# Kernel optimization log

Hardware: AMD Instinct MI355X
Metric: run time of the kernel (lower is better)

The kernel has to match this reference:

```python
import jax, jax.numpy as jnp
import numpy as np

CHEB_K = 3  # from init_kwargs


def setup_inputs() -> dict:
    key = jax.random.key(0)
    k1, k2, k3, k4 = jax.random.split(key, 4)
    B, N, C_IN, C_OUT, D = 32, 4096, 32, 64, 16
    x = jax.random.normal(k1, (B, N, C_IN), dtype=jnp.float32)
    node_embeddings = jax.random.normal(k2, (N, D), dtype=jnp.float32)
    laplacian_mx = jnp.zeros((N, N), dtype=jnp.float32)  # unused by forward
    weights_pool = jax.random.normal(k3, (D, CHEB_K, C_IN, C_OUT), dtype=jnp.float32) * 0.1
    bias_pool = jax.random.normal(k4, (D, C_OUT), dtype=jnp.float32) * 0.1
    return {
        'x': x,
        'node_embeddings': node_embeddings,
        'laplacian_mx': laplacian_mx,
        'weights_pool': weights_pool,
        'bias_pool': bias_pool,
    }


def reference(x, node_embeddings, laplacian_mx, weights_pool, bias_pool):
    N = node_embeddings.shape[0]
    # adaptive adjacency: softmax(relu(E E^T)) over rows
    supports = jax.nn.softmax(jax.nn.relu(node_embeddings @ node_embeddings.T), axis=1)
    # Chebyshev recursion T_0=I, T_1=A, T_k = 2A T_{k-1} - T_{k-2}
    support_set = [jnp.eye(N, dtype=x.dtype), supports]
    for _ in range(2, CHEB_K):
        support_set.append(2.0 * supports @ support_set[-1] - support_set[-2])
    supports_k = jnp.stack(support_set, axis=0)  # [K, N, N]
    # per-node generated weights/bias
    weights = jnp.einsum('nd,dkio->nkio', node_embeddings, weights_pool)  # [N,K,I,O]
    bias = node_embeddings @ bias_pool  # [N, O]
    # graph propagation: [K,N,N] x [B,N,I] -> [B,K,N,I] -> [B,N,K,I]
    x_g = jnp.einsum('knm,bmc->bknc', supports_k, x).transpose(0, 2, 1, 3)
    # per-node grouped GEMM
    out = jnp.einsum('bnki,nkio->bno', x_g, weights) + bias
    return out
```

## Files before the change

kernel.cpp:

```cpp
#include <hip/hip_runtime.h>
#include <hip/hip_bf16.h>

#define N_NODES 4096
#define BATCH   32
#define CIN     32
#define COUT    64
#define DEMB    16
#define NCOL    (BATCH * CIN)
#define KIO     (3 * CIN * COUT)
#define SPLITK  4

typedef __bf16 bf16x8 __attribute__((ext_vector_type(8)));
typedef float  floatx4 __attribute__((ext_vector_type(4)));

__device__ inline void load_lds16(const void* g, void* l) {
    __builtin_amdgcn_global_load_lds(
        (const __attribute__((address_space(1))) void*)g,
        (__attribute__((address_space(3))) void*)l, 16, 0, 0);
}

__global__ __launch_bounds__(256) void compute_U_kernel(
        const float* __restrict__ E, __hip_bfloat16* __restrict__ U,
        float* __restrict__ invRow) {
    const int n0   = blockIdx.x * 8;
    const int t    = threadIdx.x;
    const int lane = t & 63, wave = t >> 6;
    __shared__ float red[4][8];

    float en[8][DEMB];
#pragma unroll
    for (int r = 0; r < 8; ++r) {
        const float4* er = (const float4*)&E[(size_t)(n0 + r) * DEMB];
        const float4 a0 = er[0], a1 = er[1], a2 = er[2], a3 = er[3];
        en[r][ 0]=a0.x; en[r][ 1]=a0.y; en[r][ 2]=a0.z; en[r][ 3]=a0.w;
        en[r][ 4]=a1.x; en[r][ 5]=a1.y; en[r][ 6]=a1.z; en[r][ 7]=a1.w;
        en[r][ 8]=a2.x; en[r][ 9]=a2.y; en[r][10]=a2.z; en[r][11]=a2.w;
        en[r][12]=a3.x; en[r][13]=a3.y; en[r][14]=a3.z; en[r][15]=a3.w;
    }

    float sum[8] = {0.f, 0.f, 0.f, 0.f, 0.f, 0.f, 0.f, 0.f};

    for (int tile = 0; tile < 16; ++tile) {
        const int c = tile * 256 + t;
        const float4* em4 = (const float4*)&E[(size_t)c * DEMB];
        const float4 b0 = em4[0], b1 = em4[1], b2 = em4[2], b3 = em4[3];
        float em[DEMB];
        em[ 0]=b0.x; em[ 1]=b0.y; em[ 2]=b0.z; em[ 3]=b0.w;
        em[ 4]=b1.x; em[ 5]=b1.y; em[ 6]=b1.z; em[ 7]=b1.w;
        em[ 8]=b2.x; em[ 9]=b2.y; em[10]=b2.z; em[11]=b2.w;
        em[12]=b3.x; em[13]=b3.y; em[14]=b3.z; em[15]=b3.w;
#pragma unroll
        for (int r = 0; r < 8; ++r) {
            float dt = 0.f;
#pragma unroll
            for (int d = 0; d < DEMB; ++d) dt += en[r][d] * em[d];
            const float ev = __expf(fmaxf(dt, 0.f));
            sum[r] += ev;
            U[(size_t)(n0 + r) * N_NODES + c] = __float2bfloat16(ev);
        }
    }
#pragma unroll
    for (int r = 0; r < 8; ++r)
#pragma unroll
        for (int off = 32; off > 0; off >>= 1) sum[r] += __shfl_xor(sum[r], off);
    if (lane == 0)
#pragma unroll
        for (int r = 0; r < 8; ++r) red[wave][r] = sum[r];
    __syncthreads();
    if (t < 8)
        invRow[n0 + t] = 1.0f / (red[0][t] + red[1][t] + red[2][t] + red[3][t]);
}

__global__ __launch_bounds__(256) void transpose_kernel(
        const float* __restrict__ x,
        __hip_bfloat16* __restrict__ Xt, __hip_bfloat16* __restrict__ Bt) {
    const int m0 = blockIdx.x * 64;
    const int b  = blockIdx.y;
    const int t  = threadIdx.x;
    __shared__ float tile[64][33];
    {
        const int ml = t >> 2, cg = (t & 3) * 8;
        const float* src = &x[((size_t)b * N_NODES + (m0 + ml)) * CIN + cg];
        const float4 r0 = *(const float4*)src;
        const float4 r1 = *(const float4*)(src + 4);
        tile[ml][cg+0] = r0.x; tile[ml][cg+1] = r0.y; tile[ml][cg+2] = r0.z; tile[ml][cg+3] = r0.w;
        tile[ml][cg+4] = r1.x; tile[ml][cg+5] = r1.y; tile[ml][cg+6] = r1.z; tile[ml][cg+7] = r1.w;
    }
    __syncthreads();
    {
        const int ml = t >> 2, cg = (t & 3) * 8;
        __hip_bfloat16* dst = &Xt[(size_t)(m0 + ml) * NCOL + b * CIN + cg];
#pragma unroll
        for (int j = 0; j < 8; ++j) dst[j] = __float2bfloat16(tile[ml][cg + j]);
    }
    {
        const int c = t >> 3, mg = (t & 7) * 8;
        __hip_bfloat16* dst = &Bt[(size_t)(b * CIN + c) * N_NODES + m0 + mg];
#pragma unroll
        for (int j = 0; j < 8; ++j) dst[j] = __float2bfloat16(tile[mg + j][c]);
    }
}

__global__ __launch_bounds__(256) void gen_w_kernel(
        const float* __restrict__ E, const float* __restrict__ Wp,
        __hip_bfloat16* __restrict__ Wn) {
    const int c   = blockIdx.x >> 3;
    const int oo0 = (blockIdx.x & 7) * 8;
    const int nc  = blockIdx.y * 64;
    const int t   = threadIdx.x;
    const int kk  = t & 31;
    const int oo  = oo0 + (t >> 5);

    __shared__ float et[64][DEMB];
    ((float4*)et)[t] = ((const float4*)&E[(size_t)nc * DEMB])[t];
    __syncthreads();

    const int srccol = (c * 32 + kk) * 64 + oo;
    float w[DEMB];
#pragma unroll
    for (int d = 0; d < DEMB; ++d) w[d] = Wp[(size_t)d * KIO + srccol];

    const int dstoff = c * 2048 + (oo >> 4) * 512 + (oo & 15) * 32 + kk;
    for (int nl = 0; nl < 64; ++nl) {
        float acc = 0.0f;
#pragma unroll
        for (int d = 0; d < DEMB; ++d) acc += et[nl][d] * w[d];
        Wn[(size_t)(nc + nl) * KIO + dstoff] = __float2bfloat16(acc);
    }
}

#define GBM 256
#define GBN 256
#define GBK 64

__global__ __launch_bounds__(512, 2) void gemm_splitk_kernel(
        const __hip_bfloat16* __restrict__ A,
        const __hip_bfloat16* __restrict__ Bt,
        __hip_bfloat16* __restrict__ P,
        int M, int NC, int K) {
    const int t    = threadIdx.x;
    const int row0 = blockIdx.x * GBM;
    const int col0 = blockIdx.y * GBN;
    const int z    = blockIdx.z;
    const int NT   = (K >> 6) / SPLITK;
    const int kb0  = z * NT * GBK;

    __shared__ alignas(16) __hip_bfloat16 As[2][16384];
    __shared__ alignas(16) __hip_bfloat16 Bs[2][16384];

    const int lane = t & 63, wave = t >> 6;
    const int l16 = lane & 15, quad = lane >> 4;
    const int wr = wave >> 2, wc = wave & 3;

    const int R0 = wr * 128 + l16;
    const int C0 = wc * 64 + l16;
    const int u_par = (l16 & 1) * 4 + quad;
    const int Aoff = (R0 >> 1) * 64 + ((u_par ^ ((R0 >> 1) & 7)) * 8);
    const int Boff = (C0 >> 1) * 64 + ((u_par ^ ((C0 >> 1) & 7)) * 8);

    auto stageA = [&](int buf, int kb, int kh, int s) {
        const int L = s * 512 + t;
        const int p = L >> 3, j = L & 7;
        const int u = j ^ (p & 7);
        const int rr = p * 2 + (u >> 2);
        const int qq = u & 3;
        load_lds16(&A[(size_t)(row0 + rr) * K + kb + kh * 32 + qq * 8],
                   &As[buf][(size_t)(kh * 1024 + L) * 8]);
    };
    auto stageB = [&](int buf, int kb, int kh, int s) {
        const int L = s * 512 + t;
        const int p = L >> 3, j = L & 7;
        const int u = j ^ (p & 7);
        const int rr = p * 2 + (u >> 2);
        const int qq = u & 3;
        load_lds16(&Bt[(size_t)(col0 + rr) * K + kb + kh * 32 + qq * 8],
                   &Bs[buf][(size_t)(kh * 1024 + L) * 8]);
    };

    floatx4 acc[8][4] = {};

#pragma unroll
    for (int s = 0; s < 2; ++s) stageA(0, kb0, 0, s);
#pragma unroll
    for (int s = 0; s < 2; ++s) stageB(0, kb0, 0, s);
#pragma unroll
    for (int s = 0; s < 2; ++s) stageA(0, kb0, 1, s);
#pragma unroll
    for (int s = 0; s < 2; ++s) stageB(0, kb0, 1, s);
#pragma unroll
    for (int s = 0; s < 2; ++s) stageA(1, kb0 + GBK, 0, s);
#pragma unroll
    for (int s = 0; s < 2; ++s) stageB(1, kb0 + GBK, 0, s);
    asm volatile("s_waitcnt vmcnt(4)" ::: "memory");
    __builtin_amdgcn_s_barrier();
    __builtin_amdgcn_sched_barrier(0);

    for (int tt = 0; tt < NT; ++tt) {
        const int buf = tt & 1;
        const int nb1 = (tt + 1) & 1;
        const int nb2 = buf;
        const int kb1 = kb0 + (tt + 1) * GBK;
        const int kb2 = kb0 + (tt + 2) * GBK;
        const bool g1 = (tt + 1 < NT), g2 = (tt + 2 < NT);

        bf16x8 bfrag[4], afrag[4];

#pragma unroll
        for (int n = 0; n < 4; ++n)
            bfrag[n] = *(const bf16x8*)&Bs[buf][n * 512 + Boff];
#pragma unroll
        for (int m = 0; m < 4; ++m)
            afrag[m] = *(const bf16x8*)&As[buf][m * 512 + Aoff];
        if (g1) { stageA(nb1, kb1, 1, 0); stageA(nb1, kb1, 1, 1); }
        __builtin_amdgcn_s_barrier();
        asm volatile("s_waitcnt lgkmcnt(0)" ::: "memory");
        __builtin_amdgcn_sched_barrier(0);
        __builtin_amdgcn_s_setprio(1);
#pragma unroll
        for (int m = 0; m < 4; ++m)
#pragma unroll
            for (int n = 0; n < 4; ++n)
                acc[m][n] = __builtin_amdgcn_mfma_f32_16x16x32_bf16(
                                afrag[m], bfrag[n], acc[m][n], 0, 0, 0);
        __builtin_amdgcn_s_setprio(0);
        __builtin_amdgcn_s_barrier();

#pragma unroll
        for (int m = 0; m < 4; ++m)
            afrag[m] = *(const bf16x8*)&As[buf][2048 + m * 512 + Aoff];
        if (g1) { stageB(nb1, kb1, 1, 0); stageB(nb1, kb1, 1, 1); }
        __builtin_amdgcn_s_barrier();
        asm volatile("s_waitcnt lgkmcnt(0)" ::: "memory");
        __builtin_amdgcn_sched_barrier(0);
        __builtin_amdgcn_s_setprio(1);
#pragma unroll
        for (int m = 0; m < 4; ++m)
#pragma unroll
            for (int n = 0; n < 4; ++n)
                acc[4 + m][n] = __builtin_amdgcn_mfma_f32_16x16x32_bf16(
                                    afrag[m], bfrag[n], acc[4 + m][n], 0, 0, 0);
        __builtin_amdgcn_s_setprio(0);
        __builtin_amdgcn_s_barrier();

#pragma unroll
        for (int n = 0; n < 4; ++n)
            bfrag[n] = *(const bf16x8*)&Bs[buf][8192 + n * 512 + Boff];
#pragma unroll
        for (int m = 0; m < 4; ++m)
            afrag[m] = *(const bf16x8*)&As[buf][8192 + m * 512 + Aoff];
        if (g2) { stageA(nb2, kb2, 0, 0); stageA(nb2, kb2, 0, 1); }
        __builtin_amdgcn_s_barrier();
        asm volatile("s_waitcnt lgkmcnt(0)" ::: "memory");
        __builtin_amdgcn_sched_barrier(0);
        __builtin_amdgcn_s_setprio(1);
#pragma unroll
        for (int m = 0; m < 4; ++m)
#pragma unroll
            for (int n = 0; n < 4; ++n)
                acc[m][n] = __builtin_amdgcn_mfma_f32_16x16x32_bf16(
                                afrag[m], bfrag[n], acc[m][n], 0, 0, 0);
        __builtin_amdgcn_s_setprio(0);
        __builtin_amdgcn_s_barrier();

#pragma unroll
        for (int m = 0; m < 4; ++m)
            afrag[m] = *(const bf16x8*)&As[buf][8192 + 2048 + m * 512 + Aoff];
        if (g2) { stageB(nb2, kb2, 0, 0); stageB(nb2, kb2, 0, 1); }
        __builtin_amdgcn_s_barrier();
        asm volatile("s_waitcnt lgkmcnt(0)" ::: "memory");
        __builtin_amdgcn_sched_barrier(0);
        __builtin_amdgcn_s_setprio(1);
#pragma unroll
        for (int m = 0; m < 4; ++m)
#pragma unroll
            for (int n = 0; n < 4; ++n)
                acc[4 + m][n] = __builtin_amdgcn_mfma_f32_16x16x32_bf16(
                                    afrag[m], bfrag[n], acc[4 + m][n], 0, 0, 0);
        __builtin_amdgcn_s_setprio(0);
        if (tt < NT - 2) asm volatile("s_waitcnt vmcnt(4)" ::: "memory");
        else             asm volatile("s_waitcnt vmcnt(0)" ::: "memory");
        __builtin_amdgcn_s_barrier();
        __builtin_amdgcn_sched_barrier(0);
    }

    __hip_bfloat16* Pz = P + (size_t)z * M * NC;
#pragma unroll
    for (int mq = 0; mq < 2; ++mq)
#pragma unroll
        for (int m = 0; m < 4; ++m)
#pragma unroll
            for (int n = 0; n < 4; ++n)
#pragma unroll
                for (int r = 0; r < 4; ++r) {
                    const int rg = row0 + wr * 128 + mq * 64 + m * 16 + quad * 4 + r;
                    const int cg = col0 + wc * 64 + n * 16 + l16;
                    Pz[(size_t)rg * NC + cg] = __float2bfloat16(acc[mq * 4 + m][n][r]);
                }
}

__global__ __launch_bounds__(256) void combine1_kernel(
        const __hip_bfloat16* __restrict__ P, const float* __restrict__ invRow,
        __hip_bfloat16* __restrict__ Y, __hip_bfloat16* __restrict__ Yt,
        int M, int NC) {
    const int c0 = blockIdx.x * 64, m0 = blockIdx.y * 64;
    const int t = threadIdx.x;
    __shared__ float tile[64][65];
    const size_t stride = (size_t)M * NC;
#pragma unroll
    for (int j = 0; j < 16; ++j) {
        const int lin = t + j * 256;
        const int r = lin >> 6, c = lin & 63;
        const size_t idx = (size_t)(m0 + r) * NC + c0 + c;
        float s = 0.f;
#pragma unroll
        for (int z = 0; z < SPLITK; ++z) s += __bfloat162float(P[idx + z * stride]);
        s *= invRow[m0 + r];
        tile[r][c] = s;
        Y[idx] = __float2bfloat16(s);
    }
    __syncthreads();
#pragma unroll
    for (int j = 0; j < 16; ++j) {
        const int lin = t + j * 256;
        const int c = lin >> 6, r = lin & 63;
        Yt[(size_t)(c0 + c) * M + m0 + r] = __float2bfloat16(tile[r][c]);
    }
}

__global__ __launch_bounds__(256) void combine2_kernel(
        const __hip_bfloat16* __restrict__ P, const float* __restrict__ invRow,
        const __hip_bfloat16* __restrict__ sub, __hip_bfloat16* __restrict__ Y2,
        int M, int NC) {
    const size_t stride = (size_t)M * NC;
    const size_t idx0 = (size_t)blockIdx.x * 4096 + threadIdx.x;
#pragma unroll
    for (int j = 0; j < 16; ++j) {
        const size_t idx = idx0 + (size_t)j * 256;
        float s = 0.f;
#pragma unroll
        for (int z = 0; z < SPLITK; ++z) s += __bfloat162float(P[idx + z * stride]);
        s *= invRow[idx >> 10];
        Y2[idx] = __float2bfloat16(2.0f * s - __bfloat162float(sub[idx]));
    }
}

__global__ __launch_bounds__(256) void final_kernel(
        const __hip_bfloat16* __restrict__ Xt, const __hip_bfloat16* __restrict__ Y1,
        const __hip_bfloat16* __restrict__ Y2, const __hip_bfloat16* __restrict__ Wn,
        const float* __restrict__ E, const float* __restrict__ bias_pool,
        float* __restrict__ out) {
    const int t    = threadIdx.x;
    const int lane = t & 63, wave = t >> 6;
    const int l16  = lane & 15, quad = lane >> 4;
    const int n    = blockIdx.x * 4 + wave;

    const __hip_bfloat16* srcs[3] = {Xt, Y1, Y2};
    const __hip_bfloat16* Wnode = Wn + (size_t)n * KIO;

    floatx4 acc[2][4] = {};

#pragma unroll
    for (int c = 0; c < 3; ++c) {
        bf16x8 af[2];
#pragma unroll
        for (int mt = 0; mt < 2; ++mt)
            af[mt] = *(const bf16x8*)&srcs[c][(size_t)n * NCOL +
                                              (mt * 16 + l16) * 32 + quad * 8];
#pragma unroll
        for (int ot = 0; ot < 4; ++ot) {
            const bf16x8 bfr = *(const bf16x8*)&Wnode[(size_t)c * 2048 +
                                                      ot * 512 + l16 * 32 + quad * 8];
#pragma unroll
            for (int mt = 0; mt < 2; ++mt)
                acc[mt][ot] = __builtin_amdgcn_mfma_f32_16x16x32_bf16(
                                  af[mt], bfr, acc[mt][ot], 0, 0, 0);
        }
    }

    float en[DEMB];
#pragma unroll
    for (int d = 0; d < DEMB; ++d) en[d] = E[(size_t)n * DEMB + d];
#pragma unroll
    for (int ot = 0; ot < 4; ++ot) {
        float bv = 0.f;
        const int o = ot * 16 + l16;
#pragma unroll
        for (int d = 0; d < DEMB; ++d) bv += en[d] * bias_pool[d * COUT + o];
#pragma unroll
        for (int mt = 0; mt < 2; ++mt)
#pragma unroll
            for (int r = 0; r < 4; ++r) {
                const int b = mt * 16 + quad * 4 + r;
                out[((size_t)b * N_NODES + n) * COUT + o] = acc[mt][ot][r] + bv;
            }
    }
}

extern "C" void kernel_launch(void* const* d_in, const int* in_sizes, int n_in,
                              void* d_out, int out_size, void* d_ws, size_t ws_size,
                              hipStream_t stream) {
    (void)in_sizes; (void)n_in; (void)out_size; (void)ws_size;
    const float* x  = (const float*)d_in[0];
    const float* E  = (const float*)d_in[1];
    const float* Wp = (const float*)d_in[3];
    const float* bp = (const float*)d_in[4];
    float* out = (float*)d_out;

    char* ws = (char*)d_ws;
    __hip_bfloat16* U   = (__hip_bfloat16*)(ws);
    __hip_bfloat16* Xt  = (__hip_bfloat16*)(ws + 33554432);
    __hip_bfloat16* Bt1 = (__hip_bfloat16*)(ws + 41943040);
    __hip_bfloat16* Y1  = (__hip_bfloat16*)(ws + 50331648);
    __hip_bfloat16* Y1t = (__hip_bfloat16*)(ws + 58720256);
    __hip_bfloat16* P   = (__hip_bfloat16*)(ws + 67108864);
    float*       invRow = (float*)(ws + 100663296);
    __hip_bfloat16* Wn  = (__hip_bfloat16*)(ws + 67108864);

    compute_U_kernel<<<N_NODES / 8, 256, 0, stream>>>(E, U, invRow);
    transpose_kernel<<<dim3(N_NODES / 64, BATCH), 256, 0, stream>>>(x, Xt, Bt1);
    gemm_splitk_kernel<<<dim3(N_NODES / GBM, NCOL / GBN, SPLITK), 512, 0, stream>>>(
        U, Bt1, P, N_NODES, NCOL, N_NODES);
    combine1_kernel<<<dim3(NCOL / 64, N_NODES / 64), 256, 0, stream>>>(
        P, invRow, Y1, Y1t, N_NODES, NCOL);
    gemm_splitk_kernel<<<dim3(N_NODES / GBM, NCOL / GBN, SPLITK), 512, 0, stream>>>(
        U, Y1t, P, N_NODES, NCOL, N_NODES);
    combine2_kernel<<<dim3(N_NODES * NCOL / 4096), 256, 0, stream>>>(
        P, invRow, Xt, Bt1, N_NODES, NCOL);
    gen_w_kernel<<<dim3(24, N_NODES / 64), 256, 0, stream>>>(E, Wp, Wn);
    final_kernel<<<N_NODES / 4, 256, 0, stream>>>(Xt, Y1, Bt1, Wn, E, bp, out);
}
```

Baseline: 279.6 us.

## Drop explicit waitcnt/sched barriers and add classic double-buffered GEMM for second pass

Removes the manual lgkmcnt waits and sched_barrier fences in the pipelined split-K GEMM, leaving instruction scheduling and LDS waits to the compiler. Adds a second, simpler double-buffered GEMM kernel that prefetches the whole next K tile after a single __syncthreads per iteration, and uses it for the second propagation GEMM. The two launches are meant to compare scheduling strategies. Relying on compiler-inserted waits around asm barriers risks worse overlap, and the classic kernel has fewer barriers but less fine-grained overlap.

```diff
diff --git a/kernel.cpp b/kernel.cpp
--- a/kernel.cpp
+++ b/kernel.cpp
@@ -133,49 +133,63 @@
 #define GBN 256
 #define GBK 64
 
-__global__ __launch_bounds__(512, 2) void gemm_splitk_kernel(
+#define GEMM_PREAMBLE                                                          \
+    const int t    = threadIdx.x;                                              \
+    const int row0 = blockIdx.x * GBM;                                         \
+    const int col0 = blockIdx.y * GBN;                                         \
+    const int z    = blockIdx.z;                                               \
+    const int NT   = (K >> 6) / SPLITK;                                        \
+    const int kb0  = z * NT * GBK;                                             \
+    const int lane = t & 63, wave = t >> 6;                                    \
+    const int l16 = lane & 15, quad = lane >> 4;                               \
+    const int wr = wave >> 2, wc = wave & 3;                                   \
+    const int R0 = wr * 128 + l16;                                             \
+    const int C0 = wc * 64 + l16;                                              \
+    const int u_par = (l16 & 1) * 4 + quad;                                    \
+    const int Aoff = (R0 >> 1) * 64 + ((u_par ^ ((R0 >> 1) & 7)) * 8);         \
+    const int Boff = (C0 >> 1) * 64 + ((u_par ^ ((C0 >> 1) & 7)) * 8);         \
+    auto stageA = [&](int buf, int kb, int kh, int s) {                        \
+        const int L = s * 512 + t;                                             \
+        const int p = L >> 3, j = L & 7;                                       \
+        const int u = j ^ (p & 7);                                             \
+        const int rr = p * 2 + (u >> 2);                                       \
+        const int qq = u & 3;                                                  \
+        load_lds16(&A[(size_t)(row0 + rr) * K + kb + kh * 32 + qq * 8],        \
+                   &As[buf][(size_t)(kh * 1024 + L) * 8]);                     \
+    };                                                                         \
+    auto stageB = [&](int buf, int kb, int kh, int s) {                        \
+        const int L = s * 512 + t;                                             \
+        const int p = L >> 3, j = L & 7;                                       \
+        const int u = j ^ (p & 7);                                             \
+        const int rr = p * 2 + (u >> 2);                                       \
+        const int qq = u & 3;                                                  \
+        load_lds16(&Bt[(size_t)(col0 + rr) * K + kb + kh * 32 + qq * 8],       \
+                   &Bs[buf][(size_t)(kh * 1024 + L) * 8]);                     \
+    };
+
+#define GEMM_EPILOGUE                                                          \
+    __hip_bfloat16* Pz = P + (size_t)z * M * NC;                               \
+    _Pragma("unroll")                                                          \
+    for (int mq = 0; mq < 2; ++mq)                                             \
+        _Pragma("unroll")                                                      \
+        for (int m = 0; m < 4; ++m)                                            \
+            _Pragma("unroll")                                                  \
+            for (int n = 0; n < 4; ++n)                                        \
+                _Pragma("unroll")                                              \
+                for (int r = 0; r < 4; ++r) {                                  \
+                    const int rg = row0 + wr * 128 + mq * 64 + m * 16 + quad * 4 + r; \
+                    const int cg = col0 + wc * 64 + n * 16 + l16;              \
+                    Pz[(size_t)rg * NC + cg] = __float2bfloat16(acc[mq * 4 + m][n][r]); \
+                }
+
+__global__ __launch_bounds__(512, 2) void gemm_pipe_kernel(
         const __hip_bfloat16* __restrict__ A,
         const __hip_bfloat16* __restrict__ Bt,
         __hip_bfloat16* __restrict__ P,
         int M, int NC, int K) {
-    const int t    = threadIdx.x;
-    const int row0 = blockIdx.x * GBM;
-    const int col0 = blockIdx.y * GBN;
-    const int z    = blockIdx.z;
-    const int NT   = (K >> 6) / SPLITK;
-    const int kb0  = z * NT * GBK;
-
     __shared__ alignas(16) __hip_bfloat16 As[2][16384];
     __shared__ alignas(16) __hip_bfloat16 Bs[2][16384];
-
-    const int lane = t & 63, wave = t >> 6;
-    const int l16 = lane & 15, quad = lane >> 4;
-    const int wr = wave >> 2, wc = wave & 3;
-
-    const int R0 = wr * 128 + l16;
-    const int C0 = wc * 64 + l16;
-    const int u_par = (l16 & 1) * 4 + quad;
-    const int Aoff = (R0 >> 1) * 64 + ((u_par ^ ((R0 >> 1) & 7)) * 8);
-    const int Boff = (C0 >> 1) * 64 + ((u_par ^ ((C0 >> 1) & 7)) * 8);
-
-    auto stageA = [&](int buf, int kb, int kh, int s) {
-        const int L = s * 512 + t;
-        const int p = L >> 3, j = L & 7;
-        const int u = j ^ (p & 7);
-        const int rr = p * 2 + (u >> 2);
-        const int qq = u & 3;
-        load_lds16(&A[(size_t)(row0 + rr) * K + kb + kh * 32 + qq * 8],
-                   &As[buf][(size_t)(kh * 1024 + L) * 8]);
-    };
-    auto stageB = [&](int buf, int kb, int kh, int s) {
-        const int L = s * 512 + t;
-        const int p = L >> 3, j = L & 7;
-        const int u = j ^ (p & 7);
-        const int rr = p * 2 + (u >> 2);
-        const int qq = u & 3;
-        load_lds16(&Bt[(size_t)(col0 + rr) * K + kb + kh * 32 + qq * 8],
-                   &Bs[buf][(size_t)(kh * 1024 + L) * 8]);
-    };
+    GEMM_PREAMBLE
 
     floatx4 acc[8][4] = {};
 
@@ -193,7 +207,6 @@
     for (int s = 0; s < 2; ++s) stageB(1, kb0 + GBK, 0, s);
     asm volatile("s_waitcnt vmcnt(4)" ::: "memory");
     __builtin_amdgcn_s_barrier();
-    __builtin_amdgcn_sched_barrier(0);
 
     for (int tt = 0; tt < NT; ++tt) {
         const int buf = tt & 1;
@@ -213,8 +226,6 @@
             afrag[m] = *(const bf16x8*)&As[buf][m * 512 + Aoff];
         if (g1) { stageA(nb1, kb1, 1, 0); stageA(nb1, kb1, 1, 1); }
         __builtin_amdgcn_s_barrier();
-        asm volatile("s_waitcnt lgkmcnt(0)" ::: "memory");
-        __builtin_amdgcn_sched_barrier(0);
         __builtin_amdgcn_s_setprio(1);
 #pragma unroll
         for (int m = 0; m < 4; ++m)
@@ -230,8 +241,6 @@
             afrag[m] = *(const bf16x8*)&As[buf][2048 + m * 512 + Aoff];
         if (g1) { stageB(nb1, kb1, 1, 0); stageB(nb1, kb1, 1, 1); }
         __builtin_amdgcn_s_barrier();
-        asm volatile("s_waitcnt lgkmcnt(0)" ::: "memory");
-        __builtin_amdgcn_sched_barrier(0);
         __builtin_amdgcn_s_setprio(1);
 #pragma unroll
         for (int m = 0; m < 4; ++m)
@@ -250,8 +259,6 @@
             afrag[m] = *(const bf16x8*)&As[buf][8192 + m * 512 + Aoff];
         if (g2) { stageA(nb2, kb2, 0, 0); stageA(nb2, kb2, 0, 1); }
         __builtin_amdgcn_s_barrier();
-        asm volatile("s_waitcnt lgkmcnt(0)" ::: "memory");
-        __builtin_amdgcn_sched_barrier(0);
         __builtin_amdgcn_s_setprio(1);
 #pragma unroll
         for (int m = 0; m < 4; ++m)
@@ -267,8 +274,6 @@
             afrag[m] = *(const bf16x8*)&As[buf][8192 + 2048 + m * 512 + Aoff];
         if (g2) { stageB(nb2, kb2, 0, 0); stageB(nb2, kb2, 0, 1); }
         __builtin_amdgcn_s_barrier();
-        asm volatile("s_waitcnt lgkmcnt(0)" ::: "memory");
-        __builtin_amdgcn_sched_barrier(0);
         __builtin_amdgcn_s_setprio(1);
 #pragma unroll
         for (int m = 0; m < 4; ++m)
@@ -280,22 +285,60 @@
         if (tt < NT - 2) asm volatile("s_waitcnt vmcnt(4)" ::: "memory");
         else             asm volatile("s_waitcnt vmcnt(0)" ::: "memory");
         __builtin_amdgcn_s_barrier();
-        __builtin_amdgcn_sched_barrier(0);
-    }
-
-    __hip_bfloat16* Pz = P + (size_t)z * M * NC;
-#pragma unroll
-    for (int mq = 0; mq < 2; ++mq)
-#pragma unroll
-        for (int m = 0; m < 4; ++m)
+    }
+
+    GEMM_EPILOGUE
+}
+
+__global__ __launch_bounds__(512, 2) void gemm_classic_kernel(
+        const __hip_bfloat16* __restrict__ A,
+        const __hip_bfloat16* __restrict__ Bt,
+        __hip_bfloat16* __restrict__ P,
+        int M, int NC, int K) {
+    __shared__ alignas(16) __hip_bfloat16 As[2][16384];
+    __shared__ alignas(16) __hip_bfloat16 Bs[2][16384];
+    GEMM_PREAMBLE
+
+    floatx4 acc[8][4] = {};
+
+#pragma unroll
+    for (int kh = 0; kh < 2; ++kh)
+#pragma unroll
+        for (int s = 0; s < 2; ++s) { stageA(0, kb0, kh, s); stageB(0, kb0, kh, s); }
+
+    for (int tt = 0; tt < NT; ++tt) {
+        const int buf = tt & 1;
+        __syncthreads();
+        if (tt + 1 < NT) {
+            const int kb1 = kb0 + (tt + 1) * GBK;
+#pragma unroll
+            for (int kh = 0; kh < 2; ++kh)
+#pragma unroll
+                for (int s = 0; s < 2; ++s) { stageA(buf ^ 1, kb1, kh, s); stageB(buf ^ 1, kb1, kh, s); }
+        }
+        bf16x8 bfrag[4], afrag[4];
+#pragma unroll
+        for (int kq = 0; kq < 2; ++kq) {
+            const int kofs = kq * 8192;
 #pragma unroll
             for (int n = 0; n < 4; ++n)
-#pragma unroll
-                for (int r = 0; r < 4; ++r) {
-                    const int rg = row0 + wr * 128 + mq * 64 + m * 16 + quad * 4 + r;
-                    const int cg = col0 + wc * 64 + n * 16 + l16;
-                    Pz[(size_t)rg * NC + cg] = __float2bfloat16(acc[mq * 4 + m][n][r]);
-                }
+                bfrag[n] = *(const bf16x8*)&Bs[buf][kofs + n * 512 + Boff];
+#pragma unroll
+            for (int mq = 0; mq < 2; ++mq) {
+#pragma unroll
+                for (int m = 0; m < 4; ++m)
+                    afrag[m] = *(const bf16x8*)&As[buf][kofs + mq * 2048 + m * 512 + Aoff];
+#pragma unroll
+                for (int m = 0; m < 4; ++m)
+#pragma unroll
+                    for (int n = 0; n < 4; ++n)
+                        acc[mq * 4 + m][n] = __builtin_amdgcn_mfma_f32_16x16x32_bf16(
+                                                 afrag[m], bfrag[n], acc[mq * 4 + m][n], 0, 0, 0);
+            }
+        }
+    }
+
+    GEMM_EPILOGUE
 }
 
 __global__ __launch_bounds__(256) void combine1_kernel(
@@ -418,11 +461,11 @@
 
     compute_U_kernel<<<N_NODES / 8, 256, 0, stream>>>(E, U, invRow);
     transpose_kernel<<<dim3(N_NODES / 64, BATCH), 256, 0, stream>>>(x, Xt, Bt1);
-    gemm_splitk_kernel<<<dim3(N_NODES / GBM, NCOL / GBN, SPLITK), 512, 0, stream>>>(
+    gemm_pipe_kernel<<<dim3(N_NODES / GBM, NCOL / GBN, SPLITK), 512, 0, stream>>>(
         U, Bt1, P, N_NODES, NCOL, N_NODES);
     combine1_kernel<<<dim3(NCOL / 64, N_NODES / 64), 256, 0, stream>>>(
         P, invRow, Y1, Y1t, N_NODES, NCOL);
-    gemm_splitk_kernel<<<dim3(N_NODES / GBM, NCOL / GBN, SPLITK), 512, 0, stream>>>(
+    gemm_classic_kernel<<<dim3(N_NODES / GBM, NCOL / GBN, SPLITK), 512, 0, stream>>>(
         U, Y1t, P, N_NODES, NCOL, N_NODES);
     combine2_kernel<<<dim3(N_NODES * NCOL / 4096), 256, 0, stream>>>(
         P, invRow, Xt, Bt1, N_NODES, NCOL);
```

Result: no change. 280.5 us (+0.3%).

## Fuse second split-K combine into final kernel and retile GEMM to 128x256

Applied to the files above, without the earlier changes.

Drops the combine2 kernel. The final kernel now reads the two split-K partials, scales them by the row inverse and subtracts Xt to form Y2 in registers, which removes one full write and read of the Y2 intermediate. The split-K GEMM goes from 256x256 tiles with SPLITK 4 to 128x256 tiles with SPLITK 2, which halves the partial-sum traffic but changes the block count and per-wave MFMA work. The workspace layout is rearranged so Wn overwrites U and so partials, Y1 and Xt do not overlap. Some lgkmcnt waits and sched barriers are removed, which could affect LDS-read correctness or ordering.

```diff
diff --git a/kernel.cpp b/kernel.cpp
--- a/kernel.cpp
+++ b/kernel.cpp
@@ -8,7 +8,7 @@
 #define DEMB    16
 #define NCOL    (BATCH * CIN)
 #define KIO     (3 * CIN * COUT)
-#define SPLITK  4
+#define SPLITK  2
 
 typedef __bf16 bf16x8 __attribute__((ext_vector_type(8)));
 typedef float  floatx4 __attribute__((ext_vector_type(4)));
@@ -129,7 +129,7 @@
     }
 }
 
-#define GBM 256
+#define GBM 128
 #define GBN 256
 #define GBK 64
 
@@ -145,27 +145,27 @@
     const int NT   = (K >> 6) / SPLITK;
     const int kb0  = z * NT * GBK;
 
-    __shared__ alignas(16) __hip_bfloat16 As[2][16384];
+    __shared__ alignas(16) __hip_bfloat16 As[2][8192];
     __shared__ alignas(16) __hip_bfloat16 Bs[2][16384];
 
     const int lane = t & 63, wave = t >> 6;
     const int l16 = lane & 15, quad = lane >> 4;
     const int wr = wave >> 2, wc = wave & 3;
 
-    const int R0 = wr * 128 + l16;
+    const int R0 = wr * 64 + l16;
     const int C0 = wc * 64 + l16;
     const int u_par = (l16 & 1) * 4 + quad;
-    const int Aoff = (R0 >> 1) * 64 + ((u_par ^ ((R0 >> 1) & 7)) * 8);
-    const int Boff = (C0 >> 1) * 64 + ((u_par ^ ((C0 >> 1) & 7)) * 8);
-
-    auto stageA = [&](int buf, int kb, int kh, int s) {
-        const int L = s * 512 + t;
+    const int Abase = (R0 >> 1) * 64 + ((u_par ^ ((R0 >> 1) & 7)) * 8);
+    const int Bbase = (C0 >> 1) * 64 + ((u_par ^ ((C0 >> 1) & 7)) * 8);
+
+    auto stageA = [&](int buf, int kb, int kh) {
+        const int L = t;
         const int p = L >> 3, j = L & 7;
         const int u = j ^ (p & 7);
         const int rr = p * 2 + (u >> 2);
         const int qq = u & 3;
         load_lds16(&A[(size_t)(row0 + rr) * K + kb + kh * 32 + qq * 8],
-                   &As[buf][(size_t)(kh * 1024 + L) * 8]);
+                   &As[buf][(size_t)(kh * 4096 + L * 8)]);
     };
     auto stageB = [&](int buf, int kb, int kh, int s) {
         const int L = s * 512 + t;
@@ -174,47 +174,35 @@
         const int rr = p * 2 + (u >> 2);
         const int qq = u & 3;
         load_lds16(&Bt[(size_t)(col0 + rr) * K + kb + kh * 32 + qq * 8],
-                   &Bs[buf][(size_t)(kh * 1024 + L) * 8]);
+                   &Bs[buf][(size_t)(kh * 8192 + L * 8)]);
     };
 
-    floatx4 acc[8][4] = {};
-
-#pragma unroll
-    for (int s = 0; s < 2; ++s) stageA(0, kb0, 0, s);
-#pragma unroll
-    for (int s = 0; s < 2; ++s) stageB(0, kb0, 0, s);
-#pragma unroll
-    for (int s = 0; s < 2; ++s) stageA(0, kb0, 1, s);
-#pragma unroll
-    for (int s = 0; s < 2; ++s) stageB(0, kb0, 1, s);
-#pragma unroll
-    for (int s = 0; s < 2; ++s) stageA(1, kb0 + GBK, 0, s);
-#pragma unroll
-    for (int s = 0; s < 2; ++s) stageB(1, kb0 + GBK, 0, s);
-    asm volatile("s_waitcnt vmcnt(4)" ::: "memory");
+    floatx4 acc[4][4] = {};
+
+    stageA(0, kb0, 0); stageB(0, kb0, 0, 0); stageB(0, kb0, 0, 1);
+    stageA(0, kb0, 1); stageB(0, kb0, 1, 0); stageB(0, kb0, 1, 1);
+    stageA(1, kb0 + GBK, 0); stageB(1, kb0 + GBK, 0, 0); stageB(1, kb0 + GBK, 0, 1);
+    asm volatile("s_waitcnt vmcnt(3)" ::: "memory");
     __builtin_amdgcn_s_barrier();
-    __builtin_amdgcn_sched_barrier(0);
 
     for (int tt = 0; tt < NT; ++tt) {
         const int buf = tt & 1;
-        const int nb1 = (tt + 1) & 1;
+        const int nb1 = buf ^ 1;
         const int nb2 = buf;
         const int kb1 = kb0 + (tt + 1) * GBK;
         const int kb2 = kb0 + (tt + 2) * GBK;
         const bool g1 = (tt + 1 < NT), g2 = (tt + 2 < NT);
 
-        bf16x8 bfrag[4], afrag[4];
-
+        bf16x8 afrag[4], bfrag[4];
+
+#pragma unroll
+        for (int m = 0; m < 4; ++m)
+            afrag[m] = *(const bf16x8*)&As[buf][m * 512 + Abase];
 #pragma unroll
         for (int n = 0; n < 4; ++n)
-            bfrag[n] = *(const bf16x8*)&Bs[buf][n * 512 + Boff];
-#pragma unroll
-        for (int m = 0; m < 4; ++m)
-            afrag[m] = *(const bf16x8*)&As[buf][m * 512 + Aoff];
-        if (g1) { stageA(nb1, kb1, 1, 0); stageA(nb1, kb1, 1, 1); }
+            bfrag[n] = *(const bf16x8*)&Bs[buf][n * 512 + Bbase];
+        if (g1) { stageA(nb1, kb1, 1); stageB(nb1, kb1, 1, 0); stageB(nb1, kb1, 1, 1); }
         __builtin_amdgcn_s_barrier();
-        asm volatile("s_waitcnt lgkmcnt(0)" ::: "memory");
-        __builtin_amdgcn_sched_barrier(0);
         __builtin_amdgcn_s_setprio(1);
 #pragma unroll
         for (int m = 0; m < 4; ++m)
@@ -227,31 +215,12 @@
 
 #pragma unroll
         for (int m = 0; m < 4; ++m)
-            afrag[m] = *(const bf16x8*)&As[buf][2048 + m * 512 + Aoff];
-        if (g1) { stageB(nb1, kb1, 1, 0); stageB(nb1, kb1, 1, 1); }
+            afrag[m] = *(const bf16x8*)&As[buf][4096 + m * 512 + Abase];
+#pragma unroll
+        for (int n = 0; n < 4; ++n)
+            bfrag[n] = *(const bf16x8*)&Bs[buf][8192 + n * 512 + Bbase];
+        if (g2) { stageA(nb2, kb2, 0); stageB(nb2, kb2, 0, 0); stageB(nb2, kb2, 0, 1); }
         __builtin_amdgcn_s_barrier();
-        asm volatile("s_waitcnt lgkmcnt(0)" ::: "memory");
-        __builtin_amdgcn_sched_barrier(0);
-        __builtin_amdgcn_s_setprio(1);
-#pragma unroll
-        for (int m = 0; m < 4; ++m)
-#pragma unroll
-            for (int n = 0; n < 4; ++n)
-                acc[4 + m][n] = __builtin_amdgcn_mfma_f32_16x16x32_bf16(
-                                    afrag[m], bfrag[n], acc[4 + m][n], 0, 0, 0);
-        __builtin_amdgcn_s_setprio(0);
-        __builtin_amdgcn_s_barrier();
-
-#pragma unroll
-        for (int n = 0; n < 4; ++n)
-            bfrag[n] = *(const bf16x8*)&Bs[buf][8192 + n * 512 + Boff];
-#pragma unroll
-        for (int m = 0; m < 4; ++m)
-            afrag[m] = *(const bf16x8*)&As[buf][8192 + m * 512 + Aoff];
-        if (g2) { stageA(nb2, kb2, 0, 0); stageA(nb2, kb2, 0, 1); }
-        __builtin_amdgcn_s_barrier();
-        asm volatile("s_waitcnt lgkmcnt(0)" ::: "memory");
-        __builtin_amdgcn_sched_barrier(0);
         __builtin_amdgcn_s_setprio(1);
 #pragma unroll
         for (int m = 0; m < 4; ++m)
@@ -260,42 +229,22 @@
                 acc[m][n] = __builtin_amdgcn_mfma_f32_16x16x32_bf16(
                                 afrag[m], bfrag[n], acc[m][n], 0, 0, 0);
         __builtin_amdgcn_s_setprio(0);
-        __builtin_amdgcn_s_barrier();
-
-#pragma unroll
-        for (int m = 0; m < 4; ++m)
-            afrag[m] = *(const bf16x8*)&As[buf][8192 + 2048 + m * 512 + Aoff];
-        if (g2) { stageB(nb2, kb2, 0, 0); stageB(nb2, kb2, 0, 1); }
-        __builtin_amdgcn_s_barrier();
-        asm volatile("s_waitcnt lgkmcnt(0)" ::: "memory");
-        __builtin_amdgcn_sched_barrier(0);
-        __builtin_amdgcn_s_setprio(1);
-#pragma unroll
-        for (int m = 0; m < 4; ++m)
-#pragma unroll
-            for (int n = 0; n < 4; ++n)
-                acc[4 + m][n] = __builtin_amdgcn_mfma_f32_16x16x32_bf16(
-                                    afrag[m], bfrag[n], acc[4 + m][n], 0, 0, 0);
-        __builtin_amdgcn_s_setprio(0);
-        if (tt < NT - 2) asm volatile("s_waitcnt vmcnt(4)" ::: "memory");
+        if (tt < NT - 2) asm volatile("s_waitcnt vmcnt(3)" ::: "memory");
         else             asm volatile("s_waitcnt vmcnt(0)" ::: "memory");
         __builtin_amdgcn_s_barrier();
-        __builtin_amdgcn_sched_barrier(0);
     }
 
     __hip_bfloat16* Pz = P + (size_t)z * M * NC;
 #pragma unroll
-    for (int mq = 0; mq < 2; ++mq)
-#pragma unroll
-        for (int m = 0; m < 4; ++m)
-#pragma unroll
-            for (int n = 0; n < 4; ++n)
-#pragma unroll
-                for (int r = 0; r < 4; ++r) {
-                    const int rg = row0 + wr * 128 + mq * 64 + m * 16 + quad * 4 + r;
-                    const int cg = col0 + wc * 64 + n * 16 + l16;
-                    Pz[(size_t)rg * NC + cg] = __float2bfloat16(acc[mq * 4 + m][n][r]);
-                }
+    for (int m = 0; m < 4; ++m)
+#pragma unroll
+        for (int n = 0; n < 4; ++n)
+#pragma unroll
+            for (int r = 0; r < 4; ++r) {
+                const int rg = row0 + wr * 64 + m * 16 + quad * 4 + r;
+                const int cg = col0 + wc * 64 + n * 16 + l16;
+                Pz[(size_t)rg * NC + cg] = __float2bfloat16(acc[m][n][r]);
+            }
 }
 
 __global__ __launch_bounds__(256) void combine1_kernel(
@@ -327,26 +276,10 @@
     }
 }
 
-__global__ __launch_bounds__(256) void combine2_kernel(
-        const __hip_bfloat16* __restrict__ P, const float* __restrict__ invRow,
-        const __hip_bfloat16* __restrict__ sub, __hip_bfloat16* __restrict__ Y2,
-        int M, int NC) {
-    const size_t stride = (size_t)M * NC;
-    const size_t idx0 = (size_t)blockIdx.x * 4096 + threadIdx.x;
-#pragma unroll
-    for (int j = 0; j < 16; ++j) {
-        const size_t idx = idx0 + (size_t)j * 256;
-        float s = 0.f;
-#pragma unroll
-        for (int z = 0; z < SPLITK; ++z) s += __bfloat162float(P[idx + z * stride]);
-        s *= invRow[idx >> 10];
-        Y2[idx] = __float2bfloat16(2.0f * s - __bfloat162float(sub[idx]));
-    }
-}
-
 __global__ __launch_bounds__(256) void final_kernel(
         const __hip_bfloat16* __restrict__ Xt, const __hip_bfloat16* __restrict__ Y1,
-        const __hip_bfloat16* __restrict__ Y2, const __hip_bfloat16* __restrict__ Wn,
+        const __hip_bfloat16* __restrict__ P,  const float* __restrict__ invRow,
+        const __hip_bfloat16* __restrict__ Wn,
         const float* __restrict__ E, const float* __restrict__ bias_pool,
         float* __restrict__ out) {
     const int t    = threadIdx.x;
@@ -354,18 +287,30 @@
     const int l16  = lane & 15, quad = lane >> 4;
     const int n    = blockIdx.x * 4 + wave;
 
-    const __hip_bfloat16* srcs[3] = {Xt, Y1, Y2};
     const __hip_bfloat16* Wnode = Wn + (size_t)n * KIO;
+    const float inv = invRow[n];
+    const size_t pstride = (size_t)N_NODES * NCOL;
 
     floatx4 acc[2][4] = {};
 
+    bf16x8 afX[2], afY1[2], afY2[2];
+#pragma unroll
+    for (int mt = 0; mt < 2; ++mt) {
+        const size_t fo = (size_t)n * NCOL + (mt * 16 + l16) * 32 + quad * 8;
+        afX[mt]  = *(const bf16x8*)&Xt[fo];
+        afY1[mt] = *(const bf16x8*)&Y1[fo];
+        const bf16x8 p0 = *(const bf16x8*)&P[fo];
+        const bf16x8 p1 = *(const bf16x8*)&P[fo + pstride];
+#pragma unroll
+        for (int j = 0; j < 8; ++j) {
+            const float v = 2.0f * inv * ((float)p0[j] + (float)p1[j]) - (float)afX[mt][j];
+            afY2[mt][j] = (__bf16)v;
+        }
+    }
+
+    const bf16x8* afs[3] = {afX, afY1, afY2};
 #pragma unroll
     for (int c = 0; c < 3; ++c) {
-        bf16x8 af[2];
-#pragma unroll
-        for (int mt = 0; mt < 2; ++mt)
-            af[mt] = *(const bf16x8*)&srcs[c][(size_t)n * NCOL +
-                                              (mt * 16 + l16) * 32 + quad * 8];
 #pragma unroll
         for (int ot = 0; ot < 4; ++ot) {
             const bf16x8 bfr = *(const bf16x8*)&Wnode[(size_t)c * 2048 +
@@ -373,7 +318,7 @@
 #pragma unroll
             for (int mt = 0; mt < 2; ++mt)
                 acc[mt][ot] = __builtin_amdgcn_mfma_f32_16x16x32_bf16(
-                                  af[mt], bfr, acc[mt][ot], 0, 0, 0);
+                                  afs[c][mt], bfr, acc[mt][ot], 0, 0, 0);
         }
     }
 
@@ -407,14 +352,14 @@
     float* out = (float*)d_out;
 
     char* ws = (char*)d_ws;
-    __hip_bfloat16* U   = (__hip_bfloat16*)(ws);
-    __hip_bfloat16* Xt  = (__hip_bfloat16*)(ws + 33554432);
-    __hip_bfloat16* Bt1 = (__hip_bfloat16*)(ws + 41943040);
-    __hip_bfloat16* Y1  = (__hip_bfloat16*)(ws + 50331648);
-    __hip_bfloat16* Y1t = (__hip_bfloat16*)(ws + 58720256);
-    __hip_bfloat16* P   = (__hip_bfloat16*)(ws + 67108864);
-    float*       invRow = (float*)(ws + 100663296);
-    __hip_bfloat16* Wn  = (__hip_bfloat16*)(ws + 67108864);
+    __hip_bfloat16* U    = (__hip_bfloat16*)(ws);
+    __hip_bfloat16* Bt1  = (__hip_bfloat16*)(ws + 33554432);
+    __hip_bfloat16* Y1t  = (__hip_bfloat16*)(ws + 41943040);
+    __hip_bfloat16* P    = (__hip_bfloat16*)(ws + 50331648);
+    __hip_bfloat16* Y1   = (__hip_bfloat16*)(ws + 67108864);
+    __hip_bfloat16* Xt   = (__hip_bfloat16*)(ws + 75497472);
+    float*       invRow  = (float*)(ws + 83886080);
+    __hip_bfloat16* Wn   = (__hip_bfloat16*)(ws);
 
     compute_U_kernel<<<N_NODES / 8, 256, 0, stream>>>(E, U, invRow);
     transpose_kernel<<<dim3(N_NODES / 64, BATCH), 256, 0, stream>>>(x, Xt, Bt1);
@@ -424,8 +369,6 @@
         P, invRow, Y1, Y1t, N_NODES, NCOL);
     gemm_splitk_kernel<<<dim3(N_NODES / GBM, NCOL / GBN, SPLITK), 512, 0, stream>>>(
         U, Y1t, P, N_NODES, NCOL, N_NODES);
-    combine2_kernel<<<dim3(N_NODES * NCOL / 4096), 256, 0, stream>>>(
-        P, invRow, Xt, Bt1, N_NODES, NCOL);
     gen_w_kernel<<<dim3(24, N_NODES / 64), 256, 0, stream>>>(E, Wp, Wn);
-    final_kernel<<<N_NODES / 4, 256, 0, stream>>>(Xt, Y1, Bt1, Wn, E, bp, out);
-}
+    final_kernel<<<N_NODES / 4, 256, 0, stream>>>(Xt, Y1, P, invRow, Wn, E, bp, out);
+}
```

New measurement: 279.4 us. Within noise of the previous version (-0.0%).

## Fuse second split-K combine into final kernel and coalesce output via LDS

Applied to the files above, without the earlier changes.

Drops the combine2 kernel and reduces the four split-K bf16 partials, scales by the row inverse and applies the Chebyshev 2AY-X step inside final_kernel, so Y2 is never written to or read back from memory. The final output is staged through shared memory and written as float4 rows instead of scattered scalar stores. The workspace is relaid out so Wn reuses the U region and P persists until final_kernel. The GEMM loop also loses its explicit lgkmcnt waits and sched_barriers, leaving instruction scheduling and LDS wait placement to the compiler, which risks a worse schedule.

```diff
diff --git a/kernel.cpp b/kernel.cpp
--- a/kernel.cpp
+++ b/kernel.cpp
@@ -193,11 +193,10 @@
     for (int s = 0; s < 2; ++s) stageB(1, kb0 + GBK, 0, s);
     asm volatile("s_waitcnt vmcnt(4)" ::: "memory");
     __builtin_amdgcn_s_barrier();
-    __builtin_amdgcn_sched_barrier(0);
 
     for (int tt = 0; tt < NT; ++tt) {
         const int buf = tt & 1;
-        const int nb1 = (tt + 1) & 1;
+        const int nb1 = buf ^ 1;
         const int nb2 = buf;
         const int kb1 = kb0 + (tt + 1) * GBK;
         const int kb2 = kb0 + (tt + 2) * GBK;
@@ -213,8 +212,6 @@
             afrag[m] = *(const bf16x8*)&As[buf][m * 512 + Aoff];
         if (g1) { stageA(nb1, kb1, 1, 0); stageA(nb1, kb1, 1, 1); }
         __builtin_amdgcn_s_barrier();
-        asm volatile("s_waitcnt lgkmcnt(0)" ::: "memory");
-        __builtin_amdgcn_sched_barrier(0);
         __builtin_amdgcn_s_setprio(1);
 #pragma unroll
         for (int m = 0; m < 4; ++m)
@@ -230,8 +227,6 @@
             afrag[m] = *(const bf16x8*)&As[buf][2048 + m * 512 + Aoff];
         if (g1) { stageB(nb1, kb1, 1, 0); stageB(nb1, kb1, 1, 1); }
         __builtin_amdgcn_s_barrier();
-        asm volatile("s_waitcnt lgkmcnt(0)" ::: "memory");
-        __builtin_amdgcn_sched_barrier(0);
         __builtin_amdgcn_s_setprio(1);
 #pragma unroll
         for (int m = 0; m < 4; ++m)
@@ -250,8 +245,6 @@
             afrag[m] = *(const bf16x8*)&As[buf][8192 + m * 512 + Aoff];
         if (g2) { stageA(nb2, kb2, 0, 0); stageA(nb2, kb2, 0, 1); }
         __builtin_amdgcn_s_barrier();
-        asm volatile("s_waitcnt lgkmcnt(0)" ::: "memory");
-        __builtin_amdgcn_sched_barrier(0);
         __builtin_amdgcn_s_setprio(1);
 #pragma unroll
         for (int m = 0; m < 4; ++m)
@@ -267,8 +260,6 @@
             afrag[m] = *(const bf16x8*)&As[buf][8192 + 2048 + m * 512 + Aoff];
         if (g2) { stageB(nb2, kb2, 0, 0); stageB(nb2, kb2, 0, 1); }
         __builtin_amdgcn_s_barrier();
-        asm volatile("s_waitcnt lgkmcnt(0)" ::: "memory");
-        __builtin_amdgcn_sched_barrier(0);
         __builtin_amdgcn_s_setprio(1);
 #pragma unroll
         for (int m = 0; m < 4; ++m)
@@ -280,7 +271,6 @@
         if (tt < NT - 2) asm volatile("s_waitcnt vmcnt(4)" ::: "memory");
         else             asm volatile("s_waitcnt vmcnt(0)" ::: "memory");
         __builtin_amdgcn_s_barrier();
-        __builtin_amdgcn_sched_barrier(0);
     }
 
     __hip_bfloat16* Pz = P + (size_t)z * M * NC;
@@ -327,45 +317,46 @@
     }
 }
 
-__global__ __launch_bounds__(256) void combine2_kernel(
-        const __hip_bfloat16* __restrict__ P, const float* __restrict__ invRow,
-        const __hip_bfloat16* __restrict__ sub, __hip_bfloat16* __restrict__ Y2,
-        int M, int NC) {
-    const size_t stride = (size_t)M * NC;
-    const size_t idx0 = (size_t)blockIdx.x * 4096 + threadIdx.x;
-#pragma unroll
-    for (int j = 0; j < 16; ++j) {
-        const size_t idx = idx0 + (size_t)j * 256;
-        float s = 0.f;
-#pragma unroll
-        for (int z = 0; z < SPLITK; ++z) s += __bfloat162float(P[idx + z * stride]);
-        s *= invRow[idx >> 10];
-        Y2[idx] = __float2bfloat16(2.0f * s - __bfloat162float(sub[idx]));
-    }
-}
-
 __global__ __launch_bounds__(256) void final_kernel(
         const __hip_bfloat16* __restrict__ Xt, const __hip_bfloat16* __restrict__ Y1,
-        const __hip_bfloat16* __restrict__ Y2, const __hip_bfloat16* __restrict__ Wn,
+        const __hip_bfloat16* __restrict__ P,  const float* __restrict__ invRow,
+        const __hip_bfloat16* __restrict__ Wn,
         const float* __restrict__ E, const float* __restrict__ bias_pool,
         float* __restrict__ out) {
     const int t    = threadIdx.x;
     const int lane = t & 63, wave = t >> 6;
     const int l16  = lane & 15, quad = lane >> 4;
-    const int n    = blockIdx.x * 4 + wave;
-
-    const __hip_bfloat16* srcs[3] = {Xt, Y1, Y2};
+    const int n0   = blockIdx.x * 4;
+    const int n    = n0 + wave;
+
+    __shared__ float ost[32][4][65];
+
     const __hip_bfloat16* Wnode = Wn + (size_t)n * KIO;
+    const float inv = invRow[n];
+    const size_t pstride = (size_t)N_NODES * NCOL;
 
     floatx4 acc[2][4] = {};
 
+    bf16x8 afX[2], afY1[2], afY2[2];
+#pragma unroll
+    for (int mt = 0; mt < 2; ++mt) {
+        const size_t fo = (size_t)n * NCOL + (mt * 16 + l16) * 32 + quad * 8;
+        afX[mt]  = *(const bf16x8*)&Xt[fo];
+        afY1[mt] = *(const bf16x8*)&Y1[fo];
+        const bf16x8 p0 = *(const bf16x8*)&P[fo];
+        const bf16x8 p1 = *(const bf16x8*)&P[fo + pstride];
+        const bf16x8 p2 = *(const bf16x8*)&P[fo + 2 * pstride];
+        const bf16x8 p3 = *(const bf16x8*)&P[fo + 3 * pstride];
+#pragma unroll
+        for (int j = 0; j < 8; ++j) {
+            const float s = (float)p0[j] + (float)p1[j] + (float)p2[j] + (float)p3[j];
+            afY2[mt][j] = (__bf16)(2.0f * inv * s - (float)afX[mt][j]);
+        }
+    }
+
+    const bf16x8* afs[3] = {afX, afY1, afY2};
 #pragma unroll
     for (int c = 0; c < 3; ++c) {
-        bf16x8 af[2];
-#pragma unroll
-        for (int mt = 0; mt < 2; ++mt)
-            af[mt] = *(const bf16x8*)&srcs[c][(size_t)n * NCOL +
-                                              (mt * 16 + l16) * 32 + quad * 8];
 #pragma unroll
         for (int ot = 0; ot < 4; ++ot) {
             const bf16x8 bfr = *(const bf16x8*)&Wnode[(size_t)c * 2048 +
@@ -373,7 +364,7 @@
 #pragma unroll
             for (int mt = 0; mt < 2; ++mt)
                 acc[mt][ot] = __builtin_amdgcn_mfma_f32_16x16x32_bf16(
-                                  af[mt], bfr, acc[mt][ot], 0, 0, 0);
+                                  afs[c][mt], bfr, acc[mt][ot], 0, 0, 0);
         }
     }
 
@@ -391,8 +382,21 @@
 #pragma unroll
             for (int r = 0; r < 4; ++r) {
                 const int b = mt * 16 + quad * 4 + r;
-                out[((size_t)b * N_NODES + n) * COUT + o] = acc[mt][ot][r] + bv;
+                ost[b][wave][o] = acc[mt][ot][r] + bv;
             }
+    }
+    __syncthreads();
+
+#pragma unroll
+    for (int j = 0; j < 8; ++j) {
+        const int c  = t + j * 256;
+        const int b  = c >> 6;
+        const int rm = c & 63;
+        const int nl = rm >> 4, o4 = (rm & 15) * 4;
+        float4 v;
+        v.x = ost[b][nl][o4 + 0]; v.y = ost[b][nl][o4 + 1];
+        v.z = ost[b][nl][o4 + 2]; v.w = ost[b][nl][o4 + 3];
+        *(float4*)&out[((size_t)b * N_NODES + n0 + nl) * COUT + o4] = v;
     }
 }
 
@@ -407,14 +411,14 @@
     float* out = (float*)d_out;
 
     char* ws = (char*)d_ws;
-    __hip_bfloat16* U   = (__hip_bfloat16*)(ws);
-    __hip_bfloat16* Xt  = (__hip_bfloat16*)(ws + 33554432);
-    __hip_bfloat16* Bt1 = (__hip_bfloat16*)(ws + 41943040);
-    __hip_bfloat16* Y1  = (__hip_bfloat16*)(ws + 50331648);
-    __hip_bfloat16* Y1t = (__hip_bfloat16*)(ws + 58720256);
-    __hip_bfloat16* P   = (__hip_bfloat16*)(ws + 67108864);
-    float*       invRow = (float*)(ws + 100663296);
-    __hip_bfloat16* Wn  = (__hip_bfloat16*)(ws + 67108864);
+    __hip_bfloat16* U    = (__hip_bfloat16*)(ws);
+    __hip_bfloat16* Bt1  = (__hip_bfloat16*)(ws + 33554432);
+    __hip_bfloat16* Y1t  = (__hip_bfloat16*)(ws + 41943040);
+    __hip_bfloat16* P    = (__hip_bfloat16*)(ws + 50331648);
+    __hip_bfloat16* Y1   = (__hip_bfloat16*)(ws + 83886080);
+    __hip_bfloat16* Xt   = (__hip_bfloat16*)(ws + 92274688);
+    float*       invRow  = (float*)(ws + 100663296);
+    __hip_bfloat16* Wn   = (__hip_bfloat16*)(ws);
 
     compute_U_kernel<<<N_NODES / 8, 256, 0, stream>>>(E, U, invRow);
     transpose_kernel<<<dim3(N_NODES / 64, BATCH), 256, 0, stream>>>(x, Xt, Bt1);
@@ -424,8 +428,6 @@
         P, invRow, Y1, Y1t, N_NODES, NCOL);
     gemm_splitk_kernel<<<dim3(N_NODES / GBM, NCOL / GBN, SPLITK), 512, 0, stream>>>(
         U, Y1t, P, N_NODES, NCOL, N_NODES);
-    combine2_kernel<<<dim3(N_NODES * NCOL / 4096), 256, 0, stream>>>(
-        P, invRow, Xt, Bt1, N_NODES, NCOL);
     gen_w_kernel<<<dim3(24, N_NODES / 64), 256, 0, stream>>>(E, Wp, Wn);
-    final_kernel<<<N_NODES / 4, 256, 0, stream>>>(Xt, Y1, Bt1, Wn, E, bp, out);
-}
+    final_kernel<<<N_NODES / 4, 256, 0, stream>>>(Xt, Y1, P, invRow, Wn, E, bp, out);
+}
```

Measured after the change: 279.0 us. Within noise of the previous version (-0.2%).
